# Kernel optimization log

Hardware: AMD Instinct MI355X
Metric: run time of the kernel (lower is better)

Reference implementation:

```python
import jax, jax.numpy as jnp
import numpy as np


def _interp_linear_align_corners(w, new_len):
    """Linear (bilinear with trivial 2nd axis) interpolation along last axis,
    align_corners=True, matching torch F.interpolate. w: (..., k) -> (..., new_len)."""
    k = w.shape[-1]
    scale = (k - 1) / (new_len - 1) if new_len > 1 else 0.0
    pos = jnp.arange(new_len, dtype=w.dtype) * jnp.asarray(scale, w.dtype)
    lo = jnp.floor(pos).astype(jnp.int32)
    hi = jnp.minimum(lo + 1, k - 1)
    frac = pos - lo.astype(w.dtype)
    return w[..., lo] * (1.0 - frac) + w[..., hi] * frac


def _depthwise_conv(x, kernel, pad_h, pad_w):
    # x: (B,C,H,W), kernel: (C,1,Kh,Kw), groups=C
    C = x.shape[1]
    return jax.lax.conv_general_dilated(
        x, kernel, window_strides=(1, 1),
        padding=[(pad_h, pad_h), (pad_w, pad_w)],
        dimension_numbers=("NCHW", "OIHW", "NCHW"),
        feature_group_count=C)


def setup_inputs() -> dict:
    key = jax.random.key(0)
    k1, k2, k3, k4, k5 = jax.random.split(key, 5)
    dim, ksize = 128, 13
    B, H, W = 32, 64, 64
    fan = 1.0 / np.sqrt(ksize)  # torch Conv2d default init scale (groups=dim -> fan_in=k)
    return {
        "x": jax.random.normal(k1, (B, dim, H, W), dtype=jnp.float32),
        "h_weight": jax.random.uniform(k2, (dim, 1, ksize, 1), jnp.float32, -fan, fan),
        "w_weight": jax.random.uniform(k3, (dim, 1, 1, ksize), jnp.float32, -fan, fan),
        "h_bias": jax.random.uniform(k4, (dim,), jnp.float32, -fan, fan),
        "w_bias": jax.random.uniform(k5, (dim,), jnp.float32, -fan, fan),
    }


def reference(x, h_weight, w_weight, h_bias, w_bias):
    B, C, H, W = x.shape
    Kh, Kw = 2 * H - 1, 2 * W - 1
    # Interpolate base kernels to instance kernel sizes (align_corners=True bilinear,
    # degenerate to 1-D linear since the other spatial dim has size 1).
    hk = _interp_linear_align_corners(h_weight[:, :, :, 0], Kh)[..., None]   # (C,1,Kh,1)
    wk = _interp_linear_align_corners(w_weight[:, :, 0, :], Kw)[:, :, None]  # (C,1,1,Kw)
    y = _depthwise_conv(x, hk, H - 1, 0) + h_bias[None, :, None, None]
    y = _depthwise_conv(y, wk, 0, W - 1) + w_bias[None, :, None, None]
    return y
```

## Files before the change

### kernel.cpp

```cpp
#include <hip/hip_runtime.h>


#define STRB 72

typedef short  bfrag  __attribute__((ext_vector_type(8)));
typedef float  f32x4  __attribute__((ext_vector_type(4)));
typedef unsigned short us4 __attribute__((ext_vector_type(4)));

__device__ __forceinline__ unsigned short f2bf(float f) {
    unsigned u = __builtin_bit_cast(unsigned, f);
    u += 0x7fffu + ((u >> 16) & 1u);
    return (unsigned short)(u >> 16);
}

__global__ __launch_bounds__(256, 4)
void oversize_conv_mfma(const float* __restrict__ x,
                        const float* __restrict__ hwt,
                        const float* __restrict__ wwt,
                        const float* __restrict__ hb,
                        const float* __restrict__ wb,
                        float* __restrict__ out)
{
    __shared__ __align__(16) unsigned short Xs[64 * STRB];
    __shared__ __align__(16) unsigned short Aw[64 * STRB];
    __shared__ __align__(16) unsigned short Ah[64 * STRB];
    __shared__ __align__(16) unsigned short PT[64 * STRB];
    __shared__ float hk[128], wk[128], sw[64];

    const int tid = threadIdx.x;
    const int bc  = blockIdx.x;
    const int c   = bc & 127;
    const size_t img = (size_t)bc * 4096;

    float4 xv[4];
    const float4* xg = (const float4*)(x + img);
    #pragma unroll
    for (int i = 0; i < 4; ++i) xv[i] = xg[tid + i * 256];

    if (tid < 127) {
        const float scale = 12.0f / 126.0f;
        float pos = (float)tid * scale;
        int   lo  = (int)pos;
        float fr  = pos - (float)lo;
        int   hi  = (lo + 1 < 12) ? lo + 1 : 12;
        hk[tid] = hwt[c * 13 + lo] * (1.0f - fr) + hwt[c * 13 + hi] * fr;
        wk[tid] = wwt[c * 13 + lo] * (1.0f - fr) + wwt[c * 13 + hi] * fr;
    }
    __syncthreads();

    {
        const int row = tid >> 2;
        const int cb  = (tid & 3) * 16;
        us4 vh[4], vw[4];
        #pragma unroll
        for (int q = 0; q < 4; ++q) {
            #pragma unroll
            for (int j = 0; j < 4; ++j) {
                int col = cb + q * 4 + j;
                vh[q][j] = f2bf(hk[col - row + 63]);
                vw[q][j] = f2bf(wk[col - row + 63]);
            }
        }
        #pragma unroll
        for (int q = 0; q < 4; ++q) {
            *(us4*)&Ah[row * STRB + cb + q * 4] = vh[q];
            *(us4*)&Aw[row * STRB + cb + q * 4] = vw[q];
        }
    }
    if (tid < 64) {
        float s = 0.f;
        #pragma unroll 8
        for (int iw = 0; iw < 64; ++iw) s += wk[iw - tid + 63];
        sw[tid] = s;
    }
    #pragma unroll
    for (int i = 0; i < 4; ++i) {
        int idx = tid + i * 256;
        int row = idx >> 4;
        int col = (idx & 15) * 4;
        us4 v;
        v[0] = f2bf(xv[i].x); v[1] = f2bf(xv[i].y);
        v[2] = f2bf(xv[i].z); v[3] = f2bf(xv[i].w);
        *(us4*)&Xs[row * STRB + col] = v;
    }
    __syncthreads();

    const int wv = tid >> 6, lane = tid & 63;
    const int r = lane & 15, g = lane >> 4;

    f32x4 acc[4] = {};
    {
        bfrag a0 = *(const bfrag*)&Xs[(wv * 16 + r) * STRB + g * 8];
        bfrag a1 = *(const bfrag*)&Xs[(wv * 16 + r) * STRB + 32 + g * 8];
        #pragma unroll
        for (int nt = 0; nt < 4; ++nt) {
            bfrag b0 = *(const bfrag*)&Aw[(nt * 16 + r) * STRB + g * 8];
            bfrag b1 = *(const bfrag*)&Aw[(nt * 16 + r) * STRB + 32 + g * 8];
            acc[nt] = __builtin_amdgcn_mfma_f32_16x16x32_bf16(a0, b0, acc[nt], 0, 0, 0);
            acc[nt] = __builtin_amdgcn_mfma_f32_16x16x32_bf16(a1, b1, acc[nt], 0, 0, 0);
        }
    }
    #pragma unroll
    for (int nt = 0; nt < 4; ++nt) {
        us4 p;
        p[0] = f2bf(acc[nt][0]); p[1] = f2bf(acc[nt][1]);
        p[2] = f2bf(acc[nt][2]); p[3] = f2bf(acc[nt][3]);
        *(us4*)&PT[(nt * 16 + r) * STRB + wv * 16 + g * 4] = p;
    }
    __syncthreads();

    const float hbc = hb[c], wbc = wb[c];
    f32x4 acc2[4];
    #pragma unroll
    for (int nt = 0; nt < 4; ++nt) {
        float bv = hbc * sw[nt * 16 + r] + wbc;
        acc2[nt] = (f32x4){bv, bv, bv, bv};
    }
    {
        bfrag a0 = *(const bfrag*)&Ah[(wv * 16 + r) * STRB + g * 8];
        bfrag a1 = *(const bfrag*)&Ah[(wv * 16 + r) * STRB + 32 + g * 8];
        #pragma unroll
        for (int nt = 0; nt < 4; ++nt) {
            bfrag b0 = *(const bfrag*)&PT[(nt * 16 + r) * STRB + g * 8];
            bfrag b1 = *(const bfrag*)&PT[(nt * 16 + r) * STRB + 32 + g * 8];
            acc2[nt] = __builtin_amdgcn_mfma_f32_16x16x32_bf16(a0, b0, acc2[nt], 0, 0, 0);
            acc2[nt] = __builtin_amdgcn_mfma_f32_16x16x32_bf16(a1, b1, acc2[nt], 0, 0, 0);
        }
    }
    float* og = out + img;
    #pragma unroll
    for (int nt = 0; nt < 4; ++nt) {
        #pragma unroll
        for (int j = 0; j < 4; ++j)
            og[(size_t)(wv * 16 + g * 4 + j) * 64 + nt * 16 + r] = acc2[nt][j];
    }
}

extern "C" void kernel_launch(void* const* d_in, const int* in_sizes, int n_in,
                              void* d_out, int out_size, void* d_ws, size_t ws_size,
                              hipStream_t stream)
{
    const float* x   = (const float*)d_in[0];
    const float* hwt = (const float*)d_in[1];
    const float* wwt = (const float*)d_in[2];
    const float* hb  = (const float*)d_in[3];
    const float* wb  = (const float*)d_in[4];
    oversize_conv_mfma<<<32 * 128, 256, 0, stream>>>(x, hwt, wwt, hb, wb, (float*)d_out);
}
```

Before: 27.57 us.

## Process four batch images per block with prefetched loads and reused Toeplitz matrices

Each block now handles four images of the same channel instead of one. The interpolated Toeplitz matrices and bias terms are built once and reused, and the next image's global loads are issued before the current image's MFMA work so memory latency overlaps compute. __syncthreads is replaced by an explicit lgkmcnt wait plus s_barrier. The grid shrinks from 4096 to 1024 blocks, which cuts parallelism and adds register pressure from the prefetch buffer.

Result: faster. 25.99 us (-5.7%).

```diff
diff --git a/kernel.cpp b/kernel.cpp
--- a/kernel.cpp
+++ b/kernel.cpp
@@ -13,13 +13,18 @@
     return (unsigned short)(u >> 16);
 }
 
+__device__ __forceinline__ void lds_barrier() {
+    asm volatile("s_waitcnt lgkmcnt(0)" ::: "memory");
+    __builtin_amdgcn_s_barrier();
+}
+
 __global__ __launch_bounds__(256, 4)
-void oversize_conv_mfma(const float* __restrict__ x,
-                        const float* __restrict__ hwt,
-                        const float* __restrict__ wwt,
-                        const float* __restrict__ hb,
-                        const float* __restrict__ wb,
-                        float* __restrict__ out)
+void oversize_conv_mfma4(const float* __restrict__ x,
+                         const float* __restrict__ hwt,
+                         const float* __restrict__ wwt,
+                         const float* __restrict__ hb,
+                         const float* __restrict__ wb,
+                         float* __restrict__ out)
 {
     __shared__ __align__(16) unsigned short Xs[64 * STRB];
     __shared__ __align__(16) unsigned short Aw[64 * STRB];
@@ -28,14 +33,20 @@
     __shared__ float hk[128], wk[128], sw[64];
 
     const int tid = threadIdx.x;
-    const int bc  = blockIdx.x;
-    const int c   = bc & 127;
-    const size_t img = (size_t)bc * 4096;
+    const int c   = blockIdx.x & 127;
+    const int g4  = blockIdx.x >> 7;
+    const size_t img0      = ((size_t)(4 * g4) * 128 + c) * 4096;
+    const size_t imgStride = (size_t)128 * 4096;
+
+    const int wv = tid >> 6, lane = tid & 63;
+    const int r = lane & 15, gq = lane >> 4;
 
     float4 xv[4];
-    const float4* xg = (const float4*)(x + img);
-    #pragma unroll
-    for (int i = 0; i < 4; ++i) xv[i] = xg[tid + i * 256];
+    {
+        const float4* xg = (const float4*)(x + img0);
+        #pragma unroll
+        for (int i = 0; i < 4; ++i) xv[i] = xg[tid + i * 256];
+    }
 
     if (tid < 127) {
         const float scale = 12.0f / 126.0f;
@@ -46,25 +57,22 @@
         hk[tid] = hwt[c * 13 + lo] * (1.0f - fr) + hwt[c * 13 + hi] * fr;
         wk[tid] = wwt[c * 13 + lo] * (1.0f - fr) + wwt[c * 13 + hi] * fr;
     }
-    __syncthreads();
+    lds_barrier();
 
     {
         const int row = tid >> 2;
         const int cb  = (tid & 3) * 16;
-        us4 vh[4], vw[4];
         #pragma unroll
         for (int q = 0; q < 4; ++q) {
+            us4 vh, vw;
             #pragma unroll
             for (int j = 0; j < 4; ++j) {
                 int col = cb + q * 4 + j;
-                vh[q][j] = f2bf(hk[col - row + 63]);
-                vw[q][j] = f2bf(wk[col - row + 63]);
+                vh[j] = f2bf(hk[col - row + 63]);
+                vw[j] = f2bf(wk[col - row + 63]);
             }
-        }
-        #pragma unroll
-        for (int q = 0; q < 4; ++q) {
-            *(us4*)&Ah[row * STRB + cb + q * 4] = vh[q];
-            *(us4*)&Aw[row * STRB + cb + q * 4] = vw[q];
+            *(us4*)&Ah[row * STRB + cb + q * 4] = vh;
+            *(us4*)&Aw[row * STRB + cb + q * 4] = vw;
         }
     }
     if (tid < 64) {
@@ -83,56 +91,86 @@
         v[2] = f2bf(xv[i].z); v[3] = f2bf(xv[i].w);
         *(us4*)&Xs[row * STRB + col] = v;
     }
-    __syncthreads();
+    lds_barrier();
 
-    const int wv = tid >> 6, lane = tid & 63;
-    const int r = lane & 15, g = lane >> 4;
+    const float hbc = hb[c], wbc = wb[c];
+    float bias_nt[4];
+    #pragma unroll
+    for (int nt = 0; nt < 4; ++nt) bias_nt[nt] = hbc * sw[nt * 16 + r] + wbc;
 
-    f32x4 acc[4] = {};
-    {
-        bfrag a0 = *(const bfrag*)&Xs[(wv * 16 + r) * STRB + g * 8];
-        bfrag a1 = *(const bfrag*)&Xs[(wv * 16 + r) * STRB + 32 + g * 8];
+    float4 xn[4];
+
+    #pragma unroll
+    for (int i = 0; i < 4; ++i) {
+        if (i < 3) {
+            const float4* xg = (const float4*)(x + img0 + (size_t)(i + 1) * imgStride);
+            #pragma unroll
+            for (int q = 0; q < 4; ++q) xn[q] = xg[tid + q * 256];
+        }
+
+        f32x4 acc[4] = {};
+        {
+            bfrag a0 = *(const bfrag*)&Xs[(wv * 16 + r) * STRB + gq * 8];
+            bfrag a1 = *(const bfrag*)&Xs[(wv * 16 + r) * STRB + 32 + gq * 8];
+            #pragma unroll
+            for (int nt = 0; nt < 4; ++nt) {
+                bfrag b0 = *(const bfrag*)&Aw[(nt * 16 + r) * STRB + gq * 8];
+                bfrag b1 = *(const bfrag*)&Aw[(nt * 16 + r) * STRB + 32 + gq * 8];
+                acc[nt] = __builtin_amdgcn_mfma_f32_16x16x32_bf16(a0, b0, acc[nt], 0, 0, 0);
+                acc[nt] = __builtin_amdgcn_mfma_f32_16x16x32_bf16(a1, b1, acc[nt], 0, 0, 0);
+            }
+        }
         #pragma unroll
         for (int nt = 0; nt < 4; ++nt) {
-            bfrag b0 = *(const bfrag*)&Aw[(nt * 16 + r) * STRB + g * 8];
-            bfrag b1 = *(const bfrag*)&Aw[(nt * 16 + r) * STRB + 32 + g * 8];
-            acc[nt] = __builtin_amdgcn_mfma_f32_16x16x32_bf16(a0, b0, acc[nt], 0, 0, 0);
-            acc[nt] = __builtin_amdgcn_mfma_f32_16x16x32_bf16(a1, b1, acc[nt], 0, 0, 0);
+            us4 p;
+            p[0] = f2bf(acc[nt][0]); p[1] = f2bf(acc[nt][1]);
+            p[2] = f2bf(acc[nt][2]); p[3] = f2bf(acc[nt][3]);
+            *(us4*)&PT[(nt * 16 + r) * STRB + wv * 16 + gq * 4] = p;
         }
-    }
-    #pragma unroll
-    for (int nt = 0; nt < 4; ++nt) {
-        us4 p;
-        p[0] = f2bf(acc[nt][0]); p[1] = f2bf(acc[nt][1]);
-        p[2] = f2bf(acc[nt][2]); p[3] = f2bf(acc[nt][3]);
-        *(us4*)&PT[(nt * 16 + r) * STRB + wv * 16 + g * 4] = p;
-    }
-    __syncthreads();
+        lds_barrier();
 
-    const float hbc = hb[c], wbc = wb[c];
-    f32x4 acc2[4];
-    #pragma unroll
-    for (int nt = 0; nt < 4; ++nt) {
-        float bv = hbc * sw[nt * 16 + r] + wbc;
-        acc2[nt] = (f32x4){bv, bv, bv, bv};
-    }
-    {
-        bfrag a0 = *(const bfrag*)&Ah[(wv * 16 + r) * STRB + g * 8];
-        bfrag a1 = *(const bfrag*)&Ah[(wv * 16 + r) * STRB + 32 + g * 8];
+        f32x4 acc2[4];
         #pragma unroll
         for (int nt = 0; nt < 4; ++nt) {
-            bfrag b0 = *(const bfrag*)&PT[(nt * 16 + r) * STRB + g * 8];
-            bfrag b1 = *(const bfrag*)&PT[(nt * 16 + r) * STRB + 32 + g * 8];
-            acc2[nt] = __builtin_amdgcn_mfma_f32_16x16x32_bf16(a0, b0, acc2[nt], 0, 0, 0);
-            acc2[nt] = __builtin_amdgcn_mfma_f32_16x16x32_bf16(a1, b1, acc2[nt], 0, 0, 0);
+            float bv = bias_nt[nt];
+            acc2[nt] = (f32x4){bv, bv, bv, bv};
         }
-    }
-    float* og = out + img;
-    #pragma unroll
-    for (int nt = 0; nt < 4; ++nt) {
-        #pragma unroll
-        for (int j = 0; j < 4; ++j)
-            og[(size_t)(wv * 16 + g * 4 + j) * 64 + nt * 16 + r] = acc2[nt][j];
+        {
+            bfrag a0 = *(const bfrag*)&Ah[(wv * 16 + r) * STRB + gq * 8];
+            bfrag a1 = *(const bfrag*)&Ah[(wv * 16 + r) * STRB + 32 + gq * 8];
+            #pragma unroll
+            for (int nt = 0; nt < 4; ++nt) {
+                bfrag b0 = *(const bfrag*)&PT[(nt * 16 + r) * STRB + gq * 8];
+                bfrag b1 = *(const bfrag*)&PT[(nt * 16 + r) * STRB + 32 + gq * 8];
+                acc2[nt] = __builtin_amdgcn_mfma_f32_16x16x32_bf16(a0, b0, acc2[nt], 0, 0, 0);
+                acc2[nt] = __builtin_amdgcn_mfma_f32_16x16x32_bf16(a1, b1, acc2[nt], 0, 0, 0);
+            }
+        }
+
+        if (i < 3) {
+            #pragma unroll
+            for (int q = 0; q < 4; ++q) {
+                int idx = tid + q * 256;
+                int row = idx >> 4;
+                int col = (idx & 15) * 4;
+                us4 v;
+                v[0] = f2bf(xn[q].x); v[1] = f2bf(xn[q].y);
+                v[2] = f2bf(xn[q].z); v[3] = f2bf(xn[q].w);
+                *(us4*)&Xs[row * STRB + col] = v;
+            }
+        }
+
+        {
+            float* og = out + img0 + (size_t)i * imgStride;
+            #pragma unroll
+            for (int nt = 0; nt < 4; ++nt) {
+                #pragma unroll
+                for (int j = 0; j < 4; ++j)
+                    og[(size_t)(wv * 16 + gq * 4 + j) * 64 + nt * 16 + r] = acc2[nt][j];
+            }
+        }
+
+        lds_barrier();
     }
 }
 
@@ -145,5 +183,5 @@
     const float* wwt = (const float*)d_in[2];
     const float* hb  = (const float*)d_in[3];
     const float* wb  = (const float*)d_in[4];
-    oversize_conv_mfma<<<32 * 128, 256, 0, stream>>>(x, hwt, wwt, hb, wb, (float*)d_out);
+    oversize_conv_mfma4<<<1024, 256, 0, stream>>>(x, hwt, wwt, hb, wb, (float*)d_out);
 }
```
